# Kernel tuning notes

Hardware: AMD Instinct MI355X
Metric: run time of the kernel (lower is better)

## Reference

```python
import jax, jax.numpy as jnp
import numpy as np

N_EMBD = 1024
N_HEAD = 16


def setup_inputs() -> dict:
    key = jax.random.key(0)
    ks = jax.random.split(key, 5)
    B, T, C = 2, 2048, N_EMBD
    x = jax.random.normal(ks[0], (B, T, C), dtype=jnp.float32)
    # parameters (stored as (in, out); forward uses x @ W + b, equivalent to torch Linear)
    s1 = 1.0 / np.sqrt(C)
    W_attn = jax.random.normal(ks[1], (C, 3 * C), dtype=jnp.float32) * s1
    b_attn = jnp.zeros((3 * C,), dtype=jnp.float32)
    W_proj = jax.random.normal(ks[2], (C, C), dtype=jnp.float32) * s1
    b_proj = jnp.zeros((C,), dtype=jnp.float32)
    return {"x": x, "W_attn": W_attn, "b_attn": b_attn, "W_proj": W_proj, "b_proj": b_proj}


def reference(x, W_attn, b_attn, W_proj, b_proj):
    B, T, C = x.shape
    H = N_HEAD
    D = C // H  # head dim
    qkv = x @ W_attn + b_attn                       # [B, T, 3C]
    q, k, v = jnp.split(qkv, 3, axis=-1)
    # [B, H, T, D]
    q = q.reshape(B, T, H, D).transpose(0, 2, 1, 3)
    k = k.reshape(B, T, H, D).transpose(0, 2, 1, 3)
    v = v.reshape(B, T, H, D).transpose(0, 2, 1, 3)
    scale = 1.0 / jnp.sqrt(jnp.asarray(D, dtype=q.dtype))
    wei = jnp.einsum("bhqd,bhkd->bhqk", q, k) * scale  # [B, H, T, T]
    causal = jnp.tril(jnp.ones((T, T), dtype=bool))
    wei = jnp.where(causal[None, None, :, :], wei, -jnp.inf)
    wei = jax.nn.softmax(wei, axis=-1)
    y = jnp.einsum("bhqk,bhkd->bhqd", wei, v)          # [B, H, T, D]
    y = y.transpose(0, 2, 1, 3).reshape(B, T, C)
    return y @ W_proj + b_proj
```

## Files before the change

kernel.cpp:

```cpp
#include <hip/hip_runtime.h>
#include <hip/hip_bf16.h>

typedef __attribute__((ext_vector_type(8))) short short8;
typedef __attribute__((ext_vector_type(4))) float floatx4;
typedef __attribute__((ext_vector_type(4))) unsigned int uintx4;
#define BF16 __hip_bfloat16

__device__ __forceinline__ unsigned short f2bf(float f) {
  unsigned int u = __builtin_bit_cast(unsigned int, f);
  unsigned int r = (u + 0x7FFFu + ((u >> 16) & 1u)) >> 16;
  return (unsigned short)r;
}

__device__ __forceinline__ unsigned int cvt_pk_bf16(float lo, float hi) {
  unsigned int r;
  asm("v_cvt_pk_bf16_f32 %0, %1, %2" : "=v"(r) : "v"(lo), "v"(hi));
  return r;
}

__device__ __forceinline__ void gload_lds16(const void* g, void* l) {
  __builtin_amdgcn_global_load_lds(
      (const __attribute__((address_space(1))) unsigned int*)g,
      (__attribute__((address_space(3))) unsigned int*)l, 16, 0, 0);
}

__global__ __launch_bounds__(256)
void cvt_bf16(const float* __restrict__ in, unsigned short* __restrict__ out, int n) {
  int i = (blockIdx.x * 256 + threadIdx.x) * 8;
  if (i >= n) return;
  float4 a = *(const float4*)(in + i);
  float4 b = *(const float4*)(in + i + 4);
  short8 v;
  v[0] = (short)f2bf(a.x); v[1] = (short)f2bf(a.y);
  v[2] = (short)f2bf(a.z); v[3] = (short)f2bf(a.w);
  v[4] = (short)f2bf(b.x); v[5] = (short)f2bf(b.y);
  v[6] = (short)f2bf(b.z); v[7] = (short)f2bf(b.w);
  *(short8*)(out + i) = v;
}

__global__ __launch_bounds__(256)
void transpose_cvt(const float* __restrict__ in, unsigned short* __restrict__ out,
                   int K, int N) {
  __shared__ float tile[64][65];
  const int nb = N >> 6;
  const int tn = blockIdx.x % nb, tk = blockIdx.x / nb;
  const int n0 = tn << 6, k0 = tk << 6;
  const int tid = threadIdx.x;
#pragma unroll
  for (int c = 0; c < 4; ++c) {
    int t = tid + c * 256;
    int r = t >> 4, col = (t & 15) << 2;
    float4 v = *(const float4*)(in + (size_t)(k0 + r) * N + n0 + col);
    tile[r][col] = v.x; tile[r][col + 1] = v.y;
    tile[r][col + 2] = v.z; tile[r][col + 3] = v.w;
  }
  __syncthreads();
#pragma unroll
  for (int c = 0; c < 2; ++c) {
    int t = tid + c * 256;
    int r = t >> 3, col = (t & 7) << 3;
    short8 v;
#pragma unroll
    for (int j = 0; j < 8; ++j) v[j] = (short)f2bf(tile[col + j][r]);
    *(short8*)(out + (size_t)(n0 + r) * K + k0 + col) = v;
  }
}

template <int EPI>
__global__ __launch_bounds__(256, 2)
void gemm_bt(const BF16* __restrict__ A, const BF16* __restrict__ Bt,
             const float* __restrict__ bias, void* __restrict__ outv,
             int M, int N, int K) {
  const int tid = threadIdx.x;
  const int w = tid >> 6, l = tid & 63;
  const int lr = l & 15, lg = l >> 4;
  const int nbx = N >> 7;
  const int bm = blockIdx.x / nbx, bn = blockIdx.x % nbx;
  const int row0 = bm << 7, col0 = bn << 7;
  const int wr = (w >> 1) << 6, wc = (w & 1) << 6;

  __shared__ __align__(16) BF16 ldsA[128 * 64];
  __shared__ __align__(16) BF16 ldsB[128 * 64];

  floatx4 acc[4][4] = {};
  const int swzl = (lr & 7) << 3;

  for (int k0 = 0; k0 < K; k0 += 64) {
#pragma unroll
    for (int c = 0; c < 4; ++c) {
      int t = w * 64 + l + c * 256;
      int ar = t >> 3;
      int ch = (t & 7) ^ (ar & 7);
      gload_lds16(A + (size_t)(row0 + ar) * K + k0 + (ch << 3),
                  ldsA + w * 512 + c * 2048);
      gload_lds16(Bt + (size_t)(col0 + ar) * K + k0 + (ch << 3),
                  ldsB + w * 512 + c * 2048);
    }
    __syncthreads();
#pragma unroll
    for (int kk = 0; kk < 64; kk += 32) {
      short8 af[4], bf[4];
#pragma unroll
      for (int m = 0; m < 4; ++m)
        af[m] = *(const short8*)(ldsA + (wr + m * 16 + lr) * 64 + ((kk + lg * 8) ^ swzl));
#pragma unroll
      for (int n = 0; n < 4; ++n)
        bf[n] = *(const short8*)(ldsB + (wc + n * 16 + lr) * 64 + ((kk + lg * 8) ^ swzl));
#pragma unroll
      for (int m = 0; m < 4; ++m)
#pragma unroll
        for (int n = 0; n < 4; ++n)
          acc[m][n] = __builtin_amdgcn_mfma_f32_16x16x32_bf16(af[m], bf[n], acc[m][n], 0, 0, 0);
    }
    __syncthreads();
  }

#pragma unroll
  for (int m = 0; m < 4; ++m)
#pragma unroll
    for (int n = 0; n < 4; ++n)
#pragma unroll
      for (int j = 0; j < 4; ++j) {
        int row = row0 + wr + m * 16 + lg * 4 + j;
        int col = col0 + wc + n * 16 + lr;
        float v = acc[m][n][j] + bias[col];
        if (EPI == 0) {
          BF16* out = (BF16*)outv;
          int s = col >> 10, cc = col & 1023;
          int hh = cc >> 6, dd = cc & 63;
          int bb = row >> 11, tt = row & 2047;
          size_t addr;
          if (s == 2)
            addr = (size_t)8388608 + (((size_t)bb * 16 + hh) * 64 + dd) * 2048 + tt;
          else
            addr = (size_t)s * 4194304 + (((size_t)bb * 16 + hh) * 2048 + tt) * 64 + dd;
          out[addr] = __float2bfloat16(v);
        } else {
          float* out = (float*)outv;
          out[(size_t)row * N + col] = v;
        }
      }
}

__global__ __launch_bounds__(256, 4)
void flash_attn(const BF16* __restrict__ qkv, BF16* __restrict__ y) {
  const int T = 2048;
  const int i = blockIdx.x;
  const int xcd = i & 7, s = i >> 3;
  const int par = (s ^ (s >> 5)) & 1;
  const int rnk = ((s >> 5) << 4) | ((s & 31) >> 1);
  const int bh = xcd * 4 + (rnk & 3);
  const int hq = rnk >> 2;
  const int qt = par ? hq : (31 - hq);
  const int b = bh >> 4, h = bh & 15;
  const int q0 = qt << 6;
  const int tid = threadIdx.x, w = tid >> 6, l = tid & 63;
  const int lr = l & 15, lg = l >> 4;

  const BF16* Q  = qkv + (size_t)bh * T * 64;
  const BF16* Kp = qkv + 4194304 + (size_t)bh * T * 64;
  const BF16* Vt = qkv + 8388608 + (size_t)bh * 64 * T;

  __shared__ __align__(16) BF16 ldsK[2][4096];
  __shared__ __align__(16) BF16 ldsV[2][6144];

  const float C1 = 0.18033688011112042f;
  const float C2 = 17.312340490667562f;
  const int swzl = (lr & 7) << 3;
  const int nt = qt + 1;

  short8 qf[2];
#pragma unroll
  for (int c = 0; c < 2; ++c)
    qf[c] = *(const short8*)(Q + (size_t)(q0 + w * 16 + lr) * 64 + c * 32 + lg * 8);

  floatx4 acc_o[4] = {};
  float lsum = 0.f;

#define STAGE(JT, BUF)                                                        \
  {                                                                           \
    const int j0_ = (JT) << 6;                                                \
    _Pragma("unroll")                                                         \
    for (int c = 0; c < 2; ++c) {                                             \
      int t = w * 64 + l + c * 256;                                           \
      int r = t >> 3;                                                         \
      int ch = (t & 7) ^ (r & 7);                                             \
      gload_lds16(Kp + (size_t)(j0_ + r) * 64 + ch * 8,                       \
                  &ldsK[BUF][w * 512 + c * 2048]);                            \
      gload_lds16(Vt + (size_t)r * T + j0_ + ch * 8,                          \
                  &ldsV[BUF][w * 512 + c * 2048]);                            \
    }                                                                         \
  }

  STAGE(0, 0);

  for (int jt = 0; jt < nt; ++jt) {
    const int j0 = jt << 6;
    const int cur = jt & 1;
    if (jt + 1 < nt) {
      STAGE(jt + 1, cur ^ 1);
      asm volatile("s_waitcnt vmcnt(4)" ::: "memory");
    } else {
      asm volatile("s_waitcnt vmcnt(0)" ::: "memory");
    }
    __builtin_amdgcn_s_barrier();

    floatx4 accs[4] = {};
    __builtin_amdgcn_s_setprio(1);
#pragma unroll
    for (int c = 0; c < 2; ++c)
#pragma unroll
      for (int n = 0; n < 4; ++n) {
        short8 kf = *(const short8*)(&ldsK[cur][(n * 16 + lr) * 64 + ((c * 32 + lg * 8) ^ swzl)]);
        accs[n] = __builtin_amdgcn_mfma_f32_16x16x32_bf16(kf, qf[c], accs[n], 0, 0, 0);
      }
    __builtin_amdgcn_s_setprio(0);

    const bool diag = (jt == qt);
    const int qrow = q0 + w * 16 + lr;
#pragma unroll
    for (int n = 0; n < 4; ++n)
#pragma unroll
      for (int j = 0; j < 4; ++j) {
        float p = exp2f(fmaf(accs[n][j], C1, -C2));
        if (diag && (j0 + n * 16 + lg * 4 + j > qrow)) p = 0.f;
        lsum += p;
        accs[n][j] = p;
      }

    __builtin_amdgcn_s_setprio(1);
#pragma unroll
    for (int c = 0; c < 2; ++c) {
      unsigned int a0 = cvt_pk_bf16(accs[2 * c][0], accs[2 * c][1]);
      unsigned int b0 = cvt_pk_bf16(accs[2 * c + 1][0], accs[2 * c + 1][1]);
      unsigned int a1 = cvt_pk_bf16(accs[2 * c][2], accs[2 * c][3]);
      unsigned int b1 = cvt_pk_bf16(accs[2 * c + 1][2], accs[2 * c + 1][3]);
      asm("v_permlane32_swap_b32 %0, %1" : "+v"(a0), "+v"(b0));
      asm("v_permlane32_swap_b32 %0, %1" : "+v"(a1), "+v"(b1));
      asm("v_permlane16_swap_b32 %0, %1" : "+v"(a0), "+v"(b0));
      asm("v_permlane16_swap_b32 %0, %1" : "+v"(a1), "+v"(b1));
      uintx4 pw;
      pw[0] = a0; pw[1] = a1; pw[2] = b0; pw[3] = b1;
      short8 pf = __builtin_bit_cast(short8, pw);
#pragma unroll
      for (int n = 0; n < 4; ++n) {
        short8 vf = *(const short8*)(&ldsV[cur][(n * 16 + lr) * 64 + ((c * 32 + lg * 8) ^ swzl)]);
        acc_o[n] = __builtin_amdgcn_mfma_f32_16x16x32_bf16(pf, vf, acc_o[n], 0, 0, 0);
      }
    }
    __builtin_amdgcn_s_setprio(0);
    __builtin_amdgcn_s_barrier();
  }
#undef STAGE

  lsum += __shfl_xor(lsum, 16, 64);
  lsum += __shfl_xor(lsum, 32, 64);
  float inv_own = 1.0f / lsum;
  float inv[4];
#pragma unroll
  for (int j = 0; j < 4; ++j) inv[j] = __shfl(inv_own, lg * 4 + j, 64);
#pragma unroll
  for (int n = 0; n < 4; ++n)
#pragma unroll
    for (int j = 0; j < 4; ++j) {
      int qr = q0 + w * 16 + lg * 4 + j;
      int dd = n * 16 + lr;
      y[((size_t)b * 2048 + qr) * 1024 + h * 64 + dd] =
          __float2bfloat16(acc_o[n][j] * inv[j]);
    }
}

extern "C" void kernel_launch(void* const* d_in, const int* in_sizes, int n_in,
                              void* d_out, int out_size, void* d_ws, size_t ws_size,
                              hipStream_t stream) {
  const float* x      = (const float*)d_in[0];
  const float* W_attn = (const float*)d_in[1];
  const float* b_attn = (const float*)d_in[2];
  const float* W_proj = (const float*)d_in[3];
  const float* b_proj = (const float*)d_in[4];
  float* out = (float*)d_out;
  BF16* ws  = (BF16*)d_ws;

  BF16* xb      = ws;
  BF16* wt_attn = xb + 4194304;
  BF16* wt_proj = wt_attn + 3145728;
  BF16* qkv     = wt_proj + 1048576;
  BF16* y       = qkv + 12582912;

  hipLaunchKernelGGL(cvt_bf16, dim3(2048), dim3(256), 0, stream,
                     x, (unsigned short*)xb, 4194304);
  hipLaunchKernelGGL(transpose_cvt, dim3(48 * 16), dim3(256), 0, stream,
                     W_attn, (unsigned short*)wt_attn, 1024, 3072);
  hipLaunchKernelGGL(transpose_cvt, dim3(16 * 16), dim3(256), 0, stream,
                     W_proj, (unsigned short*)wt_proj, 1024, 1024);
  hipLaunchKernelGGL(gemm_bt<0>, dim3(32 * 24), dim3(256), 0, stream,
                     xb, wt_attn, b_attn, (void*)qkv, 4096, 3072, 1024);
  hipLaunchKernelGGL(flash_attn, dim3(1024), dim3(256), 0, stream, qkv, y);
  hipLaunchKernelGGL(gemm_bt<1>, dim3(32 * 8), dim3(256), 0, stream,
                     y, wt_proj, b_proj, (void*)out, 4096, 1024, 1024);
}
```

Measured before the change: 109.9 us.

## Split KV loop across two wave groups and pair causal query tiles per block

Each flash-attention block now has 512 threads in two 4-wave groups. The groups process alternating KV tiles of the same query tile, then merge partial outputs and row sums through LDS. Each block handles two query tiles, one long and one short (qt=31-pr, then qt=pr), to balance causal work, and the grid is halved to 512 blocks. This aims to shorten the serial KV chain per block and even out load. The cost is more LDS (64KB), extra syncthreads and a reduction step, which may lower occupancy.

New measurement: 113.7 us. 1.03x slower.

```diff
diff --git a/kernel.cpp b/kernel.cpp
--- a/kernel.cpp
+++ b/kernel.cpp
@@ -142,132 +142,164 @@
       }
 }
 
-__global__ __launch_bounds__(256, 4)
+__global__ __launch_bounds__(512, 4)
 void flash_attn(const BF16* __restrict__ qkv, BF16* __restrict__ y) {
   const int T = 2048;
   const int i = blockIdx.x;
   const int xcd = i & 7, s = i >> 3;
-  const int par = (s ^ (s >> 5)) & 1;
-  const int rnk = ((s >> 5) << 4) | ((s & 31) >> 1);
-  const int bh = xcd * 4 + (rnk & 3);
-  const int hq = rnk >> 2;
-  const int qt = par ? hq : (31 - hq);
-  const int b = bh >> 4, h = bh & 15;
-  const int q0 = qt << 6;
+  const int bh = xcd * 4 + (s & 3);
+  const int pr = s >> 2;
+  const int b = bh >> 4, hd = bh & 15;
   const int tid = threadIdx.x, w = tid >> 6, l = tid & 63;
+  const int gg = w >> 2, wl = w & 3;
   const int lr = l & 15, lg = l >> 4;
 
   const BF16* Q  = qkv + (size_t)bh * T * 64;
   const BF16* Kp = qkv + 4194304 + (size_t)bh * T * 64;
   const BF16* Vt = qkv + 8388608 + (size_t)bh * 64 * T;
 
-  __shared__ __align__(16) BF16 ldsK[2][4096];
-  __shared__ __align__(16) BF16 ldsV[2][6144];
+  __shared__ __align__(16) char smem[65536];
+  __shared__ float ldsLsum[64];
+  BF16* ldsK = (BF16*)(smem + gg * 32768);
+  BF16* ldsV = (BF16*)(smem + gg * 32768 + 16384);
 
   const float C1 = 0.18033688011112042f;
   const float C2 = 17.312340490667562f;
   const int swzl = (lr & 7) << 3;
-  const int nt = qt + 1;
-
-  short8 qf[2];
-#pragma unroll
-  for (int c = 0; c < 2; ++c)
-    qf[c] = *(const short8*)(Q + (size_t)(q0 + w * 16 + lr) * 64 + c * 32 + lg * 8);
-
-  floatx4 acc_o[4] = {};
-  float lsum = 0.f;
 
 #define STAGE(JT, BUF)                                                        \
   {                                                                           \
     const int j0_ = (JT) << 6;                                                \
     _Pragma("unroll")                                                         \
     for (int c = 0; c < 2; ++c) {                                             \
-      int t = w * 64 + l + c * 256;                                           \
+      int t = wl * 64 + l + c * 256;                                          \
       int r = t >> 3;                                                         \
       int ch = (t & 7) ^ (r & 7);                                             \
       gload_lds16(Kp + (size_t)(j0_ + r) * 64 + ch * 8,                       \
-                  &ldsK[BUF][w * 512 + c * 2048]);                            \
+                  ldsK + (BUF) * 4096 + wl * 512 + c * 2048);                 \
       gload_lds16(Vt + (size_t)r * T + j0_ + ch * 8,                          \
-                  &ldsV[BUF][w * 512 + c * 2048]);                            \
+                  ldsV + (BUF) * 4096 + wl * 512 + c * 2048);                 \
     }                                                                         \
   }
 
-  STAGE(0, 0);
-
-  for (int jt = 0; jt < nt; ++jt) {
-    const int j0 = jt << 6;
-    const int cur = jt & 1;
-    if (jt + 1 < nt) {
-      STAGE(jt + 1, cur ^ 1);
-      asm volatile("s_waitcnt vmcnt(4)" ::: "memory");
-    } else {
-      asm volatile("s_waitcnt vmcnt(0)" ::: "memory");
-    }
-    __builtin_amdgcn_s_barrier();
-
-    floatx4 accs[4] = {};
-    __builtin_amdgcn_s_setprio(1);
+  for (int ph = 0; ph < 2; ++ph) {
+    const int qt = ph ? pr : 31 - pr;
+    const int n = qt + 1;
+    const int q0 = qt << 6;
+    const int iters = (n + 1) >> 1;
+
+    short8 qf[2];
 #pragma unroll
     for (int c = 0; c < 2; ++c)
-#pragma unroll
-      for (int n = 0; n < 4; ++n) {
-        short8 kf = *(const short8*)(&ldsK[cur][(n * 16 + lr) * 64 + ((c * 32 + lg * 8) ^ swzl)]);
-        accs[n] = __builtin_amdgcn_mfma_f32_16x16x32_bf16(kf, qf[c], accs[n], 0, 0, 0);
+      qf[c] = *(const short8*)(Q + (size_t)(q0 + wl * 16 + lr) * 64 + c * 32 + lg * 8);
+
+    floatx4 acc_o[4] = {};
+    float lsum = 0.f;
+
+    if (ph == 0) STAGE(gg, 0);
+
+    for (int it = 0; it < iters; ++it) {
+      const int jt = 2 * it + gg;
+      const int cur = (it + ph) & 1;
+      const int nx = jt + 2;
+      if (nx < n) {
+        STAGE(nx, cur ^ 1);
+        asm volatile("s_waitcnt vmcnt(4)" ::: "memory");
+      } else {
+        asm volatile("s_waitcnt vmcnt(0)" ::: "memory");
       }
-    __builtin_amdgcn_s_setprio(0);
-
-    const bool diag = (jt == qt);
-    const int qrow = q0 + w * 16 + lr;
-#pragma unroll
-    for (int n = 0; n < 4; ++n)
-#pragma unroll
-      for (int j = 0; j < 4; ++j) {
-        float p = exp2f(fmaf(accs[n][j], C1, -C2));
-        if (diag && (j0 + n * 16 + lg * 4 + j > qrow)) p = 0.f;
-        lsum += p;
-        accs[n][j] = p;
+      __builtin_amdgcn_s_barrier();
+
+      if (jt < n) {
+        const int j0 = jt << 6;
+        floatx4 accs[4] = {};
+        __builtin_amdgcn_s_setprio(1);
+#pragma unroll
+        for (int c = 0; c < 2; ++c)
+#pragma unroll
+          for (int n4 = 0; n4 < 4; ++n4) {
+            short8 kf = *(const short8*)(ldsK + cur * 4096 + (n4 * 16 + lr) * 64 +
+                                         ((c * 32 + lg * 8) ^ swzl));
+            accs[n4] = __builtin_amdgcn_mfma_f32_16x16x32_bf16(kf, qf[c], accs[n4], 0, 0, 0);
+          }
+        __builtin_amdgcn_s_setprio(0);
+
+        const bool diag = (jt == qt);
+        const int qrow = q0 + wl * 16 + lr;
+#pragma unroll
+        for (int n4 = 0; n4 < 4; ++n4)
+#pragma unroll
+          for (int j = 0; j < 4; ++j) {
+            float p = exp2f(fmaf(accs[n4][j], C1, -C2));
+            if (diag && (j0 + n4 * 16 + lg * 4 + j > qrow)) p = 0.f;
+            lsum += p;
+            accs[n4][j] = p;
+          }
+
+        __builtin_amdgcn_s_setprio(1);
+#pragma unroll
+        for (int c = 0; c < 2; ++c) {
+          unsigned int a0 = cvt_pk_bf16(accs[2 * c][0], accs[2 * c][1]);
+          unsigned int b0 = cvt_pk_bf16(accs[2 * c + 1][0], accs[2 * c + 1][1]);
+          unsigned int a1 = cvt_pk_bf16(accs[2 * c][2], accs[2 * c][3]);
+          unsigned int b1 = cvt_pk_bf16(accs[2 * c + 1][2], accs[2 * c + 1][3]);
+          asm("v_permlane32_swap_b32 %0, %1" : "+v"(a0), "+v"(b0));
+          asm("v_permlane32_swap_b32 %0, %1" : "+v"(a1), "+v"(b1));
+          asm("v_permlane16_swap_b32 %0, %1" : "+v"(a0), "+v"(b0));
+          asm("v_permlane16_swap_b32 %0, %1" : "+v"(a1), "+v"(b1));
+          uintx4 pw;
+          pw[0] = a0; pw[1] = a1; pw[2] = b0; pw[3] = b1;
+          short8 pf = __builtin_bit_cast(short8, pw);
+#pragma unroll
+          for (int n4 = 0; n4 < 4; ++n4) {
+            short8 vf = *(const short8*)(ldsV + cur * 4096 + (n4 * 16 + lr) * 64 +
+                                         ((c * 32 + lg * 8) ^ swzl));
+            acc_o[n4] = __builtin_amdgcn_mfma_f32_16x16x32_bf16(pf, vf, acc_o[n4], 0, 0, 0);
+          }
+        }
+        __builtin_amdgcn_s_setprio(0);
       }
-
-    __builtin_amdgcn_s_setprio(1);
-#pragma unroll
-    for (int c = 0; c < 2; ++c) {
-      unsigned int a0 = cvt_pk_bf16(accs[2 * c][0], accs[2 * c][1]);
-      unsigned int b0 = cvt_pk_bf16(accs[2 * c + 1][0], accs[2 * c + 1][1]);
-      unsigned int a1 = cvt_pk_bf16(accs[2 * c][2], accs[2 * c][3]);
-      unsigned int b1 = cvt_pk_bf16(accs[2 * c + 1][2], accs[2 * c + 1][3]);
-      asm("v_permlane32_swap_b32 %0, %1" : "+v"(a0), "+v"(b0));
-      asm("v_permlane32_swap_b32 %0, %1" : "+v"(a1), "+v"(b1));
-      asm("v_permlane16_swap_b32 %0, %1" : "+v"(a0), "+v"(b0));
-      asm("v_permlane16_swap_b32 %0, %1" : "+v"(a1), "+v"(b1));
-      uintx4 pw;
-      pw[0] = a0; pw[1] = a1; pw[2] = b0; pw[3] = b1;
-      short8 pf = __builtin_bit_cast(short8, pw);
-#pragma unroll
-      for (int n = 0; n < 4; ++n) {
-        short8 vf = *(const short8*)(&ldsV[cur][(n * 16 + lr) * 64 + ((c * 32 + lg * 8) ^ swzl)]);
-        acc_o[n] = __builtin_amdgcn_mfma_f32_16x16x32_bf16(pf, vf, acc_o[n], 0, 0, 0);
-      }
-    }
-    __builtin_amdgcn_s_setprio(0);
-    __builtin_amdgcn_s_barrier();
+      __builtin_amdgcn_s_barrier();
+    }
+
+    __syncthreads();
+    if (ph == 0) STAGE(gg, 1);
+    lsum += __shfl_xor(lsum, 16, 64);
+    lsum += __shfl_xor(lsum, 32, 64);
+    if (gg == 1) {
+      if (lg == 0) ldsLsum[wl * 16 + lr] = lsum;
+#pragma unroll
+      for (int n4 = 0; n4 < 4; ++n4)
+#pragma unroll
+        for (int j = 0; j < 4; ++j) {
+          int row = wl * 16 + lg * 4 + j;
+          int col = (n4 * 16 + lr) ^ (((row >> 2) & 3) << 4);
+          float* mp = (float*)(smem + 32768 + (row & 32) * 512);
+          mp[(row & 31) * 64 + col] = acc_o[n4][j];
+        }
+    }
+    __syncthreads();
+    if (gg == 0) {
+      float tot = lsum + ldsLsum[wl * 16 + lr];
+      float inv_own = 1.0f / tot;
+      float inv[4];
+#pragma unroll
+      for (int j = 0; j < 4; ++j) inv[j] = __shfl(inv_own, lg * 4 + j, 64);
+#pragma unroll
+      for (int n4 = 0; n4 < 4; ++n4)
+#pragma unroll
+        for (int j = 0; j < 4; ++j) {
+          int row = wl * 16 + lg * 4 + j;
+          int col = (n4 * 16 + lr) ^ (((row >> 2) & 3) << 4);
+          float* mp = (float*)(smem + 32768 + (row & 32) * 512);
+          float v = acc_o[n4][j] + mp[(row & 31) * 64 + col];
+          y[((size_t)b * 2048 + q0 + row) * 1024 + hd * 64 + n4 * 16 + lr] =
+              __float2bfloat16(v * inv[j]);
+        }
+    }
+    __syncthreads();
   }
 #undef STAGE
-
-  lsum += __shfl_xor(lsum, 16, 64);
-  lsum += __shfl_xor(lsum, 32, 64);
-  float inv_own = 1.0f / lsum;
-  float inv[4];
-#pragma unroll
-  for (int j = 0; j < 4; ++j) inv[j] = __shfl(inv_own, lg * 4 + j, 64);
-#pragma unroll
-  for (int n = 0; n < 4; ++n)
-#pragma unroll
-    for (int j = 0; j < 4; ++j) {
-      int qr = q0 + w * 16 + lg * 4 + j;
-      int dd = n * 16 + lr;
-      y[((size_t)b * 2048 + qr) * 1024 + h * 64 + dd] =
-          __float2bfloat16(acc_o[n][j] * inv[j]);
-    }
 }
 
 extern "C" void kernel_launch(void* const* d_in, const int* in_sizes, int n_in,
@@ -295,7 +327,7 @@
                      W_proj, (unsigned short*)wt_proj, 1024, 1024);
   hipLaunchKernelGGL(gemm_bt<0>, dim3(32 * 24), dim3(256), 0, stream,
                      xb, wt_attn, b_attn, (void*)qkv, 4096, 3072, 1024);
-  hipLaunchKernelGGL(flash_attn, dim3(1024), dim3(256), 0, stream, qkv, y);
+  hipLaunchKernelGGL(flash_attn, dim3(512), dim3(512), 0, stream, qkv, y);
   hipLaunchKernelGGL(gemm_bt<1>, dim3(32 * 8), dim3(256), 0, stream,
                      y, wt_proj, b_proj, (void*)out, 4096, 1024, 1024);
 }
```

## Split attention KV tiles across two blocks and merge partials in separate kernel

Applied to the files above, without the earlier changes.

Each query tile's causal KV range is split by tile parity across two blocks, doubling the grid to 2048 blocks. Each block writes unnormalized fp32 partial outputs and row sums to workspace, and a new merge kernel adds the halves, normalizes, and writes bf16 y. The kernel also drops the XCD-aware block ordering, raises occupancy to 5 blocks by shrinking the V LDS buffer, and confines the causal mask to the diagonal tile. It targets load imbalance and low parallelism in the longest query tiles, at the cost of an extra launch and fp32 partial traffic. The softmax uses a fixed offset with no running max, so adding the two halves stays exact.

Result: slower. 113.4 us (+3.2%).

```diff
diff --git a/kernel.cpp b/kernel.cpp
--- a/kernel.cpp
+++ b/kernel.cpp
@@ -142,32 +142,31 @@
       }
 }
 
-__global__ __launch_bounds__(256, 4)
-void flash_attn(const BF16* __restrict__ qkv, BF16* __restrict__ y) {
+__global__ __launch_bounds__(256, 5)
+void flash_attn(const BF16* __restrict__ qkv, float* __restrict__ PO,
+                float* __restrict__ PL) {
   const int T = 2048;
-  const int i = blockIdx.x;
-  const int xcd = i & 7, s = i >> 3;
-  const int par = (s ^ (s >> 5)) & 1;
-  const int rnk = ((s >> 5) << 4) | ((s & 31) >> 1);
-  const int bh = xcd * 4 + (rnk & 3);
-  const int hq = rnk >> 2;
-  const int qt = par ? hq : (31 - hq);
-  const int b = bh >> 4, h = bh & 15;
+  const int bid = blockIdx.x;
+  const int J = bid >> 5;
+  const int bh = bid & 31;
+  const int qt = 31 - (J >> 1);
+  const int par = J & 1;
   const int q0 = qt << 6;
+  const int n = qt + 1;
+  const int iters = (n - par + 1) >> 1;
   const int tid = threadIdx.x, w = tid >> 6, l = tid & 63;
   const int lr = l & 15, lg = l >> 4;
 
-  const BF16* Q  = qkv + (size_t)bh * T * 64;
-  const BF16* Kp = qkv + 4194304 + (size_t)bh * T * 64;
-  const BF16* Vt = qkv + 8388608 + (size_t)bh * 64 * T;
+  const BF16* Q  = qkv + (size_t)bh * (T * 64);
+  const BF16* Kp = qkv + 4194304 + (size_t)bh * (T * 64);
+  const BF16* Vt = qkv + 8388608 + (size_t)bh * (64 * T);
 
   __shared__ __align__(16) BF16 ldsK[2][4096];
-  __shared__ __align__(16) BF16 ldsV[2][6144];
+  __shared__ __align__(16) BF16 ldsV[2][4096];
 
   const float C1 = 0.18033688011112042f;
   const float C2 = 17.312340490667562f;
   const int swzl = (lr & 7) << 3;
-  const int nt = qt + 1;
 
   short8 qf[2];
 #pragma unroll
@@ -175,99 +174,128 @@
     qf[c] = *(const short8*)(Q + (size_t)(q0 + w * 16 + lr) * 64 + c * 32 + lg * 8);
 
   floatx4 acc_o[4] = {};
-  float lsum = 0.f;
-
-#define STAGE(JT, BUF)                                                        \
+  floatx4 lsum4 = {0.f, 0.f, 0.f, 0.f};
+
+  const int t0 = w * 64 + l, t1 = t0 + 256;
+  const int r0 = t0 >> 3, ch0 = (t0 & 7) ^ (r0 & 7);
+  const int r1 = t1 >> 3, ch1 = (t1 & 7) ^ (r1 & 7);
+  const BF16* kg0 = Kp + (((size_t)(par * 64 + r0)) << 6) + ch0 * 8;
+  const BF16* kg1 = Kp + (((size_t)(par * 64 + r1)) << 6) + ch1 * 8;
+  const BF16* vg0 = Vt + (size_t)r0 * T + par * 64 + ch0 * 8;
+  const BF16* vg1 = Vt + (size_t)r1 * T + par * 64 + ch1 * 8;
+
+#define STAGE2(BUF)                                           \
+  {                                                           \
+    gload_lds16(kg0, &ldsK[BUF][w * 512]);                    \
+    gload_lds16(vg0, &ldsV[BUF][w * 512]);                    \
+    gload_lds16(kg1, &ldsK[BUF][w * 512 + 2048]);             \
+    gload_lds16(vg1, &ldsV[BUF][w * 512 + 2048]);             \
+    kg0 += 8192; kg1 += 8192; vg0 += 128; vg1 += 128;         \
+  }
+
+#define TILE(IT, MASKED)                                                      \
   {                                                                           \
-    const int j0_ = (JT) << 6;                                                \
+    const int cur_ = (IT) & 1;                                                \
+    if ((IT) + 1 < iters) {                                                   \
+      STAGE2(cur_ ^ 1);                                                       \
+      asm volatile("s_waitcnt vmcnt(4)" ::: "memory");                        \
+    } else {                                                                  \
+      asm volatile("s_waitcnt vmcnt(0)" ::: "memory");                        \
+    }                                                                         \
+    __builtin_amdgcn_s_barrier();                                             \
+    floatx4 accs[4] = {};                                                     \
+    __builtin_amdgcn_s_setprio(1);                                            \
+    _Pragma("unroll")                                                         \
+    for (int c = 0; c < 2; ++c)                                               \
+      _Pragma("unroll")                                                       \
+      for (int n4 = 0; n4 < 4; ++n4) {                                        \
+        short8 kf = *(const short8*)(&ldsK[cur_][(n4 * 16 + lr) * 64 +        \
+                                                ((c * 32 + lg * 8) ^ swzl)]); \
+        accs[n4] = __builtin_amdgcn_mfma_f32_16x16x32_bf16(kf, qf[c], accs[n4], 0, 0, 0); \
+      }                                                                       \
+    __builtin_amdgcn_s_setprio(0);                                            \
+    _Pragma("unroll")                                                         \
+    for (int n4 = 0; n4 < 4; ++n4)                                            \
+      _Pragma("unroll")                                                       \
+      for (int j = 0; j < 4; ++j) {                                           \
+        float p = exp2f(fmaf(accs[n4][j], C1, -C2));                          \
+        if (MASKED && (n4 * 16 + lg * 4 + j > w * 16 + lr)) p = 0.f;          \
+        lsum4[j] += p;                                                        \
+        accs[n4][j] = p;                                                      \
+      }                                                                       \
+    __builtin_amdgcn_s_setprio(1);                                            \
     _Pragma("unroll")                                                         \
     for (int c = 0; c < 2; ++c) {                                             \
-      int t = w * 64 + l + c * 256;                                           \
-      int r = t >> 3;                                                         \
-      int ch = (t & 7) ^ (r & 7);                                             \
-      gload_lds16(Kp + (size_t)(j0_ + r) * 64 + ch * 8,                       \
-                  &ldsK[BUF][w * 512 + c * 2048]);                            \
-      gload_lds16(Vt + (size_t)r * T + j0_ + ch * 8,                          \
-                  &ldsV[BUF][w * 512 + c * 2048]);                            \
+      unsigned int a0 = cvt_pk_bf16(accs[2 * c][0], accs[2 * c][1]);          \
+      unsigned int b0 = cvt_pk_bf16(accs[2 * c + 1][0], accs[2 * c + 1][1]);  \
+      unsigned int a1 = cvt_pk_bf16(accs[2 * c][2], accs[2 * c][3]);          \
+      unsigned int b1 = cvt_pk_bf16(accs[2 * c + 1][2], accs[2 * c + 1][3]);  \
+      asm("v_permlane32_swap_b32 %0, %1" : "+v"(a0), "+v"(b0));               \
+      asm("v_permlane32_swap_b32 %0, %1" : "+v"(a1), "+v"(b1));               \
+      asm("v_permlane16_swap_b32 %0, %1" : "+v"(a0), "+v"(b0));               \
+      asm("v_permlane16_swap_b32 %0, %1" : "+v"(a1), "+v"(b1));               \
+      uintx4 pw; pw[0] = a0; pw[1] = a1; pw[2] = b0; pw[3] = b1;              \
+      short8 pf = __builtin_bit_cast(short8, pw);                             \
+      _Pragma("unroll")                                                       \
+      for (int n4 = 0; n4 < 4; ++n4) {                                        \
+        short8 vf = *(const short8*)(&ldsV[cur_][(n4 * 16 + lr) * 64 +        \
+                                                ((c * 32 + lg * 8) ^ swzl)]); \
+        acc_o[n4] = __builtin_amdgcn_mfma_f32_16x16x32_bf16(pf, vf, acc_o[n4], 0, 0, 0); \
+      }                                                                       \
     }                                                                         \
-  }
-
-  STAGE(0, 0);
-
-  for (int jt = 0; jt < nt; ++jt) {
-    const int j0 = jt << 6;
-    const int cur = jt & 1;
-    if (jt + 1 < nt) {
-      STAGE(jt + 1, cur ^ 1);
-      asm volatile("s_waitcnt vmcnt(4)" ::: "memory");
-    } else {
-      asm volatile("s_waitcnt vmcnt(0)" ::: "memory");
-    }
-    __builtin_amdgcn_s_barrier();
-
-    floatx4 accs[4] = {};
-    __builtin_amdgcn_s_setprio(1);
-#pragma unroll
-    for (int c = 0; c < 2; ++c)
-#pragma unroll
-      for (int n = 0; n < 4; ++n) {
-        short8 kf = *(const short8*)(&ldsK[cur][(n * 16 + lr) * 64 + ((c * 32 + lg * 8) ^ swzl)]);
-        accs[n] = __builtin_amdgcn_mfma_f32_16x16x32_bf16(kf, qf[c], accs[n], 0, 0, 0);
-      }
-    __builtin_amdgcn_s_setprio(0);
-
-    const bool diag = (jt == qt);
-    const int qrow = q0 + w * 16 + lr;
-#pragma unroll
-    for (int n = 0; n < 4; ++n)
-#pragma unroll
-      for (int j = 0; j < 4; ++j) {
-        float p = exp2f(fmaf(accs[n][j], C1, -C2));
-        if (diag && (j0 + n * 16 + lg * 4 + j > qrow)) p = 0.f;
-        lsum += p;
-        accs[n][j] = p;
-      }
-
-    __builtin_amdgcn_s_setprio(1);
-#pragma unroll
-    for (int c = 0; c < 2; ++c) {
-      unsigned int a0 = cvt_pk_bf16(accs[2 * c][0], accs[2 * c][1]);
-      unsigned int b0 = cvt_pk_bf16(accs[2 * c + 1][0], accs[2 * c + 1][1]);
-      unsigned int a1 = cvt_pk_bf16(accs[2 * c][2], accs[2 * c][3]);
-      unsigned int b1 = cvt_pk_bf16(accs[2 * c + 1][2], accs[2 * c + 1][3]);
-      asm("v_permlane32_swap_b32 %0, %1" : "+v"(a0), "+v"(b0));
-      asm("v_permlane32_swap_b32 %0, %1" : "+v"(a1), "+v"(b1));
-      asm("v_permlane16_swap_b32 %0, %1" : "+v"(a0), "+v"(b0));
-      asm("v_permlane16_swap_b32 %0, %1" : "+v"(a1), "+v"(b1));
-      uintx4 pw;
-      pw[0] = a0; pw[1] = a1; pw[2] = b0; pw[3] = b1;
-      short8 pf = __builtin_bit_cast(short8, pw);
-#pragma unroll
-      for (int n = 0; n < 4; ++n) {
-        short8 vf = *(const short8*)(&ldsV[cur][(n * 16 + lr) * 64 + ((c * 32 + lg * 8) ^ swzl)]);
-        acc_o[n] = __builtin_amdgcn_mfma_f32_16x16x32_bf16(pf, vf, acc_o[n], 0, 0, 0);
-      }
-    }
-    __builtin_amdgcn_s_setprio(0);
-    __builtin_amdgcn_s_barrier();
-  }
-#undef STAGE
-
+    __builtin_amdgcn_s_setprio(0);                                            \
+    __builtin_amdgcn_s_barrier();                                             \
+  }
+
+  const int full = iters - ((par == (qt & 1)) ? 1 : 0);
+  if (iters > 0) {
+    STAGE2(0);
+    for (int it = 0; it < full; ++it) TILE(it, false);
+    if (full < iters) TILE(full, true);
+  }
+#undef TILE
+#undef STAGE2
+
+  const int slot = (bh * 32 + qt) * 2 + par;
+  float lsum = (lsum4[0] + lsum4[1]) + (lsum4[2] + lsum4[3]);
   lsum += __shfl_xor(lsum, 16, 64);
   lsum += __shfl_xor(lsum, 32, 64);
-  float inv_own = 1.0f / lsum;
-  float inv[4];
-#pragma unroll
-  for (int j = 0; j < 4; ++j) inv[j] = __shfl(inv_own, lg * 4 + j, 64);
-#pragma unroll
-  for (int n = 0; n < 4; ++n)
-#pragma unroll
-    for (int j = 0; j < 4; ++j) {
-      int qr = q0 + w * 16 + lg * 4 + j;
-      int dd = n * 16 + lr;
-      y[((size_t)b * 2048 + qr) * 1024 + h * 64 + dd] =
-          __float2bfloat16(acc_o[n][j] * inv[j]);
-    }
+  if (lg == 0) PL[slot * 64 + w * 16 + lr] = lsum;
+  float* po = PO + (size_t)slot * 4096;
+#pragma unroll
+  for (int n4 = 0; n4 < 4; ++n4)
+#pragma unroll
+    for (int j = 0; j < 4; ++j)
+      po[(w * 16 + lg * 4 + j) * 64 + n4 * 16 + lr] = acc_o[n4][j];
+}
+
+__global__ __launch_bounds__(256)
+void attn_merge(const float* __restrict__ PO, const float* __restrict__ PL,
+                BF16* __restrict__ y) {
+  const int g = blockIdx.x * 256 + threadIdx.x;
+  const int qi = g >> 9;
+  const int rem = (g & 511) << 3;
+  const int r = rem >> 6, d0 = rem & 63;
+  const float* A = PO + (size_t)qi * 8192 + rem;
+  const float* B = A + 4096;
+  const float lA = PL[qi * 128 + r];
+  const float lB = PL[qi * 128 + 64 + r];
+  const float inv = 1.0f / (lA + lB);
+  float4 a0 = *(const float4*)A, a1 = *(const float4*)(A + 4);
+  float4 b0 = *(const float4*)B, b1 = *(const float4*)(B + 4);
+  const int bh = qi >> 5, qt = qi & 31;
+  const int b = bh >> 4, h = bh & 15;
+  const int t = qt * 64 + r;
+  short8 v;
+  v[0] = (short)f2bf((a0.x + b0.x) * inv);
+  v[1] = (short)f2bf((a0.y + b0.y) * inv);
+  v[2] = (short)f2bf((a0.z + b0.z) * inv);
+  v[3] = (short)f2bf((a0.w + b0.w) * inv);
+  v[4] = (short)f2bf((a1.x + b1.x) * inv);
+  v[5] = (short)f2bf((a1.y + b1.y) * inv);
+  v[6] = (short)f2bf((a1.z + b1.z) * inv);
+  v[7] = (short)f2bf((a1.w + b1.w) * inv);
+  *(short8*)(y + ((size_t)b * 2048 + t) * 1024 + h * 64 + d0) = v;
 }
 
 extern "C" void kernel_launch(void* const* d_in, const int* in_sizes, int n_in,
@@ -286,6 +314,8 @@
   BF16* wt_proj = wt_attn + 3145728;
   BF16* qkv     = wt_proj + 1048576;
   BF16* y       = qkv + 12582912;
+  float* PO     = (float*)(y + 4194304);
+  float* PL     = PO + 8388608;
 
   hipLaunchKernelGGL(cvt_bf16, dim3(2048), dim3(256), 0, stream,
                      x, (unsigned short*)xb, 4194304);
@@ -295,7 +325,8 @@
                      W_proj, (unsigned short*)wt_proj, 1024, 1024);
   hipLaunchKernelGGL(gemm_bt<0>, dim3(32 * 24), dim3(256), 0, stream,
                      xb, wt_attn, b_attn, (void*)qkv, 4096, 3072, 1024);
-  hipLaunchKernelGGL(flash_attn, dim3(1024), dim3(256), 0, stream, qkv, y);
+  hipLaunchKernelGGL(flash_attn, dim3(2048), dim3(256), 0, stream, qkv, PO, PL);
+  hipLaunchKernelGGL(attn_merge, dim3(2048), dim3(256), 0, stream, PO, PL, y);
   hipLaunchKernelGGL(gemm_bt<1>, dim3(32 * 8), dim3(256), 0, stream,
                      y, wt_proj, b_proj, (void*)out, 4096, 1024, 1024);
 }
```
